# Optimization experiments

Hardware: AMD Instinct MI355X
Metric: run time of the kernel (lower is better)

## Reference

```python
import jax, jax.numpy as jnp
import numpy as np

RADIUS = 2                 # soft detection radius (init kwarg)
NMS_RADIUS = 2             # hardcoded in detect_keypoints: simple_nms(scores, 2)
TOP_K = 4096
TEMPERATURE = 0.1
KSIZE = 2 * RADIUS + 1     # 5
KK = KSIZE * KSIZE         # 25


def _hw_grid(dtype):
    # flatten order j = dy*KSIZE + dx ; entry = (x_off, y_off)  (torch's [:, [1,0]])
    lin = jnp.linspace(-RADIUS, RADIUS, KSIZE, dtype=dtype)
    gx, gy = jnp.meshgrid(lin, lin)  # 'xy': gx[dy,dx]=lin[dx], gy[dy,dx]=lin[dy]
    return jnp.stack([gx, gy], axis=-1).reshape(-1, 2)  # (KK, 2)


def _maxpool(x, r):
    k = 2 * r + 1
    return jax.lax.reduce_window(x, -jnp.inf, jax.lax.max,
                                 (1, 1, k, k), (1, 1, 1, 1),
                                 ((0, 0), (0, 0), (r, r), (r, r)))


def _simple_nms(scores, r):
    zeros = jnp.zeros_like(scores)
    max_mask = scores == _maxpool(scores, r)
    for _ in range(2):
        supp_mask = _maxpool(max_mask.astype(scores.dtype), r) > 0
        supp_scores = jnp.where(supp_mask, zeros, scores)
        new_max_mask = supp_scores == _maxpool(supp_scores, r)
        max_mask = max_mask | (new_max_mask & ~supp_mask)
    return jnp.where(max_mask, scores, zeros)


def _bilinear_zeros(img, xy):
    # img: (h, w); xy: (K, 2) normalized [-1,1]; align_corners=True, zero padding
    h, w = img.shape
    px = (xy[:, 0] + 1.0) * 0.5 * (w - 1)
    py = (xy[:, 1] + 1.0) * 0.5 * (h - 1)
    x0 = jnp.floor(px); y0 = jnp.floor(py)
    wx1 = px - x0; wx0 = 1.0 - wx1
    wy1 = py - y0; wy0 = 1.0 - wy1
    def tap(xi, yi, wgt):
        valid = (xi >= 0) & (xi < w) & (yi >= 0) & (yi < h)
        xc = jnp.clip(xi, 0, w - 1).astype(jnp.int32)
        yc = jnp.clip(yi, 0, h - 1).astype(jnp.int32)
        return jnp.where(valid, img[yc, xc], 0.0) * wgt
    return (tap(x0, y0, wx0 * wy0) + tap(x0 + 1, y0, wx1 * wy0)
            + tap(x0, y0 + 1, wx0 * wy1) + tap(x0 + 1, y0 + 1, wx1 * wy1))


def _dkd_forward(scores_map):
    b, c, h, w = scores_map.shape
    dtype = scores_map.dtype
    scores_nograd = jax.lax.stop_gradient(scores_map)

    nms_scores = _simple_nms(scores_nograd, NMS_RADIUS)
    # zero out border band of width RADIUS
    ybad = (jnp.arange(h) < RADIUS) | (jnp.arange(h) >= h - RADIUS)
    xbad = (jnp.arange(w) < RADIUS) | (jnp.arange(w) >= w - RADIUS)
    border = ybad[:, None] | xbad[None, :]
    nms_scores = jnp.where(border[None, None], 0.0, nms_scores)

    # top-k over flattened score map (per image)
    _, idx = jax.lax.top_k(nms_scores.reshape(b, -1), TOP_K)  # (b, K)
    ix = idx % w
    iy = idx // w

    # patch gather == unfold(scores_map) + gather, done sparsely with zero pad
    padded = jnp.pad(scores_map[:, 0], ((0, 0), (RADIUS, RADIUS), (RADIUS, RADIUS)))
    off = jnp.arange(KSIZE)
    ys = iy[:, :, None] + off[None, None, :]           # (b, K, KSIZE)
    xs = ix[:, :, None] + off[None, None, :]
    bidx = jnp.arange(b)[:, None, None, None]
    patch_scores = padded[bidx, ys[:, :, :, None], xs[:, :, None, :]]  # (b,K,KSIZE,KSIZE)
    patch_scores = patch_scores.reshape(b, TOP_K, KK)

    hw_grid = _hw_grid(dtype)                          # (KK, 2)
    max_v = jax.lax.stop_gradient(patch_scores.max(axis=-1, keepdims=True))
    x_exp = jnp.exp((patch_scores - max_v) / TEMPERATURE)   # (b,K,KK)
    x_exp_sum = x_exp.sum(axis=-1, keepdims=True)            # (b,K,1)
    xy_residual = jnp.einsum('bkp,pd->bkd', x_exp, hw_grid) / x_exp_sum  # (b,K,2)
    hw_dist2 = (((hw_grid[None, None] - xy_residual[:, :, None]) / RADIUS) ** 2).sum(-1)
    scoredispersity = (x_exp * hw_dist2).sum(-1) / x_exp_sum[..., 0]     # (b,K)

    keypoints_xy_nms = jnp.stack([ix, iy], axis=-1).astype(dtype)
    wh = jnp.array([w - 1, h - 1], dtype=dtype)
    keypoints_xy = (keypoints_xy_nms + xy_residual) / wh * 2.0 - 1.0     # (b,K,2)

    kptscore = jax.vmap(_bilinear_zeros)(scores_map[:, 0], keypoints_xy)  # (b,K)
    return keypoints_xy, kptscore, scoredispersity


def setup_inputs() -> dict:
    key = jax.random.key(0)
    scores_map = jax.random.uniform(key, (8, 1, 1024, 1024), dtype=jnp.float32)
    return {"scores_map": scores_map}


def reference(scores_map):
    # matches torch forward: (keypoints, kptscores, scoredispersitys)
    return _dkd_forward(scores_map)
```

## Files before the change

### kernel.cpp

```cpp
#include <hip/hip_runtime.h>
#include <stdint.h>

namespace {

constexpr int B = 8;
constexpr int H = 1024;
constexpr int W = 1024;
constexpr int TOPK = 4096;
constexpr int CAND_CAP = 131072;
constexpr int SEL_CAP = 16384;
constexpr int LIST_CAP = 320;
constexpr int HIST_N = 32768;
constexpr int NCHUNK = 32;
constexpr int NHB = 48;

constexpr int RROWS = 92;
constexpr int NG = 22;
constexpr int STR = 88;
constexpr int MW4 = 4;
constexpr int NSTRIP = 11;
constexpr int NUNIT = NG * NSTRIP;

constexpr int RK_ME = 256;
constexpr int RK_CH = 1024;

constexpr size_t OFF_CNT   = 0;
constexpr size_t OFF_GHIST = 4096;
constexpr size_t OFF_RANK  = OFF_GHIST + (size_t)B * HIST_N * 4;
constexpr size_t OFF_SEL   = OFF_RANK + (size_t)B * SEL_CAP * 4;
constexpr size_t OFF_TOPK  = OFF_SEL + (size_t)B * SEL_CAP * 8;
constexpr size_t OFF_CAND  = OFF_TOPK + (size_t)B * TOPK * 8;
constexpr size_t MEMSET_BYTES = OFF_RANK + (size_t)B * SEL_CAP * 4;

__device__ __forceinline__ float max5(float a, float b, float c, float d, float e) {
  return fmaxf(fmaxf(fmaxf(a, b), fmaxf(c, d)), e);
}
__device__ __forceinline__ float4 ld4(const float* p) {
  return *reinterpret_cast<const float4*>(p);
}

template <int PASS>
__device__ __forceinline__ void score_pass(
    int u, int x0, int y0, const float* __restrict__ S,
    const uint32_t* __restrict__ SUP, uint32_t* __restrict__ MA,
    uint64_t* list, uint32_t* cnt_loc, uint64_t* cand, uint32_t* cand_count, int b) {
  const int G = u % NG, s = u / NG;
  const int r0 = 2 + 8 * s;
  const int gx0 = x0 - 12 + 4 * G;
  uint32_t colm = 0;
#pragma unroll
  for (int j = 0; j < 4; ++j)
    if ((unsigned)(gx0 + j) < (unsigned)W) colm |= 1u << j;
  const int p = 4 * G - 4;
  const int pw = (p < 0) ? 0 : (p >> 5);
  const int psh = (p < 0) ? 0 : (p & 31);
  const int pls = (p < 0) ? -p : 0;

  float4 hw[5], cw[5];
  uint32_t sn[5];
#pragma unroll
  for (int k = 0; k < 12; ++k) {
    const int rr = r0 - 2 + k;
    const float* rowp = S + rr * STR + 4 * G;
    float4 d = ld4(rowp);
    float4 a = (G > 0) ? ld4(rowp - 4) : d;
    float4 e = (G < NG - 1) ? ld4(rowp + 4) : d;
    uint32_t supn = 0;
    if (PASS != 0) {
      const uint32_t* srow = SUP + rr * MW4;
      uint64_t X = (uint64_t)srow[pw] | ((uint64_t)srow[pw + 1] << 32);
      uint64_t win = pls ? (X << pls) : (X >> psh);
      if (win & 0x001u) a.x = 0.f;
      if (win & 0x002u) a.y = 0.f;
      if (win & 0x004u) a.z = 0.f;
      if (win & 0x008u) a.w = 0.f;
      if (win & 0x010u) d.x = 0.f;
      if (win & 0x020u) d.y = 0.f;
      if (win & 0x040u) d.z = 0.f;
      if (win & 0x080u) d.w = 0.f;
      if (win & 0x100u) e.x = 0.f;
      if (win & 0x200u) e.y = 0.f;
      if (win & 0x400u) e.z = 0.f;
      if (win & 0x800u) e.w = 0.f;
      supn = (uint32_t)(win >> 4) & 0xFu;
    }
    float4 hm;
    hm.x = max5(a.z, a.w, d.x, d.y, d.z);
    hm.y = max5(a.w, d.x, d.y, d.z, d.w);
    hm.z = max5(d.x, d.y, d.z, d.w, e.x);
    hm.w = max5(d.y, d.z, d.w, e.x, e.y);
    hw[k % 5] = hm;
    cw[k % 5] = d;
    sn[k % 5] = supn;
    if (k >= 4) {
      const int rq = r0 + k - 4;
      const int gy = y0 - 12 + rq;
      float4 vm;
      vm.x = max5(hw[0].x, hw[1].x, hw[2].x, hw[3].x, hw[4].x);
      vm.y = max5(hw[0].y, hw[1].y, hw[2].y, hw[3].y, hw[4].y);
      vm.z = max5(hw[0].z, hw[1].z, hw[2].z, hw[3].z, hw[4].z);
      vm.w = max5(hw[0].w, hw[1].w, hw[2].w, hw[3].w, hw[4].w);
      float4 c = cw[(k + 3) % 5];
      uint32_t nm = (uint32_t)(c.x == vm.x) | ((uint32_t)(c.y == vm.y) << 1) |
                    ((uint32_t)(c.z == vm.z) << 2) | ((uint32_t)(c.w == vm.w) << 3);
      nm &= ((unsigned)gy < (unsigned)H) ? colm : 0u;
      const int widx = rq * MW4 + (G >> 3);
      const int shift = 4 * (G & 7);
      if (PASS == 0) {
        if (nm) atomicOr(&MA[widx], nm << shift);
      } else if (PASS == 1) {
        uint32_t v = nm & ~sn[(k + 3) % 5];
        if (v) atomicOr(&MA[widx], v << shift);
      } else {
        uint32_t fin = ((MA[widx] >> shift) & 0xFu) | (nm & ~sn[(k + 3) % 5]);
        if (fin && G >= 3 && G < 19 && rq >= 12 && rq < 76 && gy >= 2 && gy < H - 2) {
#pragma unroll
          for (int j = 0; j < 4; ++j) {
            if ((fin >> j) & 1u) {
              int gx = gx0 + j;
              if (gx >= 2 && gx < W - 2) {
                float sval = S[rq * STR + 4 * G + j];
                if (sval > 0.0f) {
                  uint32_t bits = __float_as_uint(sval);
                  uint32_t flat = (uint32_t)(gy * W + gx);
                  uint64_t key = ((uint64_t)bits << 32) | (uint64_t)(0xFFFFFFFFu - flat);
                  uint32_t pos = atomicAdd(cnt_loc, 1u);
                  if (pos < (uint32_t)LIST_CAP) {
                    list[pos] = key;
                  } else {
                    uint32_t pp = atomicAdd(&cand_count[b], 1u);
                    if (pp < (uint32_t)CAND_CAP) cand[(size_t)b * CAND_CAP + pp] = key;
                  }
                }
              }
            }
          }
        }
      }
    }
  }
}

__device__ __forceinline__ void dilate_pass(int u, int x0, int y0,
                                            const uint32_t* __restrict__ MIN_,
                                            uint32_t* __restrict__ SOUT) {
  const int G = u % NG, s = u / NG;
  const int r0 = 2 + 8 * s;
  const int gx0 = x0 - 12 + 4 * G;
  uint32_t colm = 0;
#pragma unroll
  for (int j = 0; j < 4; ++j)
    if ((unsigned)(gx0 + j) < (unsigned)W) colm |= 1u << j;
  const int p = 4 * G - 2;
  const int pw = (p < 0) ? 0 : (p >> 5);
  const int psh = (p < 0) ? 0 : (p & 31);
  const int pls = (p < 0) ? -p : 0;
  uint32_t ring[5];
#pragma unroll
  for (int k = 0; k < 12; ++k) {
    const int rr = r0 - 2 + k;
    const uint32_t* srow = MIN_ + rr * MW4;
    uint64_t X = (uint64_t)srow[pw] | ((uint64_t)srow[pw + 1] << 32);
    uint64_t win = pls ? (X << pls) : (X >> psh);
    uint64_t t = win | (win >> 1) | (win >> 2) | (win >> 3) | (win >> 4);
    ring[k % 5] = (uint32_t)t & 0xFu;
    if (k >= 4) {
      const int rq = r0 + k - 4;
      const int gy = y0 - 12 + rq;
      uint32_t nib = ring[0] | ring[1] | ring[2] | ring[3] | ring[4];
      nib &= ((unsigned)gy < (unsigned)H) ? colm : 0u;
      if (nib) atomicOr(&SOUT[rq * MW4 + (G >> 3)], nib << (4 * (G & 7)));
    }
  }
}

__global__ void __launch_bounds__(256, 4) k_nms(const float* __restrict__ scores,
                                                uint64_t* __restrict__ cand,
                                                uint32_t* __restrict__ cand_count) {
  __shared__ float S[RROWS * STR];
  __shared__ uint32_t MAs[RROWS * MW4];
  __shared__ uint32_t SP1[RROWS * MW4];
  __shared__ uint32_t SP2[RROWS * MW4];
  __shared__ uint64_t list[LIST_CAP];
  __shared__ uint32_t cnt_loc, base_g;
  const int b = blockIdx.z;
  const int x0 = blockIdx.x * 64, y0 = blockIdx.y * 64;
  const int tid = threadIdx.x;
  const float* img = scores + (size_t)b * H * W;
  if (tid == 0) cnt_loc = 0;

  for (int u = tid; u < RROWS * NG; u += 256) {
    int r = u / NG, G = u % NG;
    int gy = y0 - 12 + r, gx = x0 - 12 + 4 * G;
    float4 v;
    if ((unsigned)gy < (unsigned)H && (unsigned)gx < (unsigned)W)
      v = ld4(img + (size_t)gy * W + gx);
    else
      v = make_float4(-INFINITY, -INFINITY, -INFINITY, -INFINITY);
    *reinterpret_cast<float4*>(&S[r * STR + 4 * G]) = v;
  }
  for (int i = tid; i < RROWS * MW4; i += 256) {
    MAs[i] = 0;
    SP1[i] = 0;
    SP2[i] = 0;
  }
  __syncthreads();
  if (tid < NUNIT)
    score_pass<0>(tid, x0, y0, S, nullptr, MAs, nullptr, nullptr, nullptr, nullptr, b);
  __syncthreads();
  if (tid < NUNIT) dilate_pass(tid, x0, y0, MAs, SP1);
  __syncthreads();
  if (tid < NUNIT)
    score_pass<1>(tid, x0, y0, S, SP1, MAs, nullptr, nullptr, nullptr, nullptr, b);
  __syncthreads();
  if (tid < NUNIT) dilate_pass(tid, x0, y0, MAs, SP2);
  __syncthreads();
  if (tid < NUNIT)
    score_pass<2>(tid, x0, y0, S, SP2, MAs, list, &cnt_loc, cand, cand_count, b);
  __syncthreads();
  uint32_t nblk = cnt_loc;
  uint32_t nmain = nblk < (uint32_t)LIST_CAP ? nblk : (uint32_t)LIST_CAP;
  if (tid == 0) base_g = atomicAdd(&cand_count[b], nmain);
  __syncthreads();
  uint32_t bg = base_g;
  for (uint32_t i = tid; i < nmain; i += 256) {
    uint32_t pp = bg + i;
    if (pp < (uint32_t)CAND_CAP) cand[(size_t)b * CAND_CAP + pp] = list[i];
  }
}

__global__ void __launch_bounds__(256) k_hist(const uint64_t* __restrict__ cand,
                                              const uint32_t* __restrict__ cand_count,
                                              uint32_t* __restrict__ ghist) {
  const int b = blockIdx.y;
  uint32_t n = cand_count[b];
  if (n > (uint32_t)CAND_CAP) n = CAND_CAP;
  uint32_t* gh = ghist + (size_t)b * HIST_N;
  const uint64_t* cb = cand + (size_t)b * CAND_CAP;
  const int lane = threadIdx.x & 63;
  for (uint32_t i = blockIdx.x * 256 + threadIdx.x;; i += NHB * 256) {
    bool valid = i < n;
    uint64_t act = __ballot(valid);
    if (!act) break;
    uint32_t bkt = 0;
    if (valid) bkt = (uint32_t)(cb[i] >> 47);
    uint64_t peers = act;
#pragma unroll
    for (int bit = 0; bit < 15; ++bit) {
      uint64_t bb = __ballot((bkt >> bit) & 1u);
      peers &= ((bkt >> bit) & 1u) ? bb : ~bb;
    }
    if (valid && (__ffsll((unsigned long long)peers) - 1) == lane)
      atomicAdd(&gh[bkt], (uint32_t)__popcll((unsigned long long)peers));
  }
}

__global__ void __launch_bounds__(256) k_chunksum(const uint32_t* __restrict__ ghist,
                                                  uint32_t* __restrict__ gchunk) {
  const int b = blockIdx.y, c = blockIdx.x;
  const uint32_t* gh = ghist + (size_t)b * HIST_N + c * 1024;
  uint32_t s = 0;
#pragma unroll
  for (int j = 0; j < 4; ++j) s += gh[threadIdx.x + 256 * j];
#pragma unroll
  for (int m = 1; m < 64; m <<= 1) s += __shfl_xor(s, m);
  __shared__ uint32_t red[4];
  if ((threadIdx.x & 63) == 0) red[threadIdx.x >> 6] = s;
  __syncthreads();
  if (threadIdx.x == 0) gchunk[b * NCHUNK + c] = red[0] + red[1] + red[2] + red[3];
}

__global__ void __launch_bounds__(1024) k_findthr(const uint32_t* __restrict__ ghist,
                                                  const uint32_t* __restrict__ gchunk,
                                                  uint64_t* __restrict__ thr_key) {
  __shared__ uint32_t ch[NCHUNK];
  __shared__ uint32_t h[1024];
  __shared__ int shCC;
  __shared__ uint32_t sh_above;
  const int b = blockIdx.x, t = threadIdx.x;
  if (t < NCHUNK) ch[t] = gchunk[b * NCHUNK + t];
  __syncthreads();
  if (t == 0) {
    uint32_t run = 0;
    int CC = -1;
    uint32_t above = 0;
    for (int c = NCHUNK - 1; c >= 0; --c) {
      uint32_t nrun = run + ch[c];
      if (run < (uint32_t)TOPK && nrun >= (uint32_t)TOPK) { CC = c; above = run; }
      run = nrun;
    }
    if (run < (uint32_t)TOPK) CC = -1;
    shCC = CC;
    sh_above = above;
  }
  __syncthreads();
  const int CC = shCC;
  if (CC < 0) {
    if (t == 0) thr_key[b] = 0ull;
    return;
  }
  const uint32_t above = sh_above;
  h[t] = ghist[(size_t)b * HIST_N + CC * 1024 + t];
  __syncthreads();
  for (int d = 1; d < 1024; d <<= 1) {
    uint32_t v = (t + d < 1024) ? h[t + d] : 0u;
    __syncthreads();
    h[t] += v;
    __syncthreads();
  }
  uint32_t cum = above + h[t];
  uint32_t cumn = (t + 1 < 1024) ? above + h[t + 1] : above;
  if (cum >= (uint32_t)TOPK && cumn < (uint32_t)TOPK)
    thr_key[b] = (uint64_t)(CC * 1024 + t) << 47;
}

__global__ void __launch_bounds__(1024) k_compact(const uint64_t* __restrict__ cand,
                                                  const uint32_t* __restrict__ cand_count,
                                                  const uint64_t* __restrict__ thr_key,
                                                  uint64_t* __restrict__ sel,
                                                  uint32_t* __restrict__ sel_count) {
  __shared__ uint64_t list[1024];
  __shared__ uint32_t cnt_loc;
  __shared__ uint32_t base_g;
  const int b = blockIdx.y;
  uint32_t n = cand_count[b];
  if (n > (uint32_t)CAND_CAP) n = CAND_CAP;
  const int tid = threadIdx.x;
  if (tid == 0) cnt_loc = 0;
  __syncthreads();
  uint32_t i = blockIdx.x * 1024 + tid;
  if (i < n) {
    uint64_t key = cand[(size_t)b * CAND_CAP + i];
    if (key >= thr_key[b]) {
      uint32_t pos = atomicAdd(&cnt_loc, 1u);
      list[pos] = key;
    }
  }
  __syncthreads();
  uint32_t nblk = cnt_loc;
  if (tid == 0 && nblk > 0) base_g = atomicAdd(&sel_count[b], nblk);
  __syncthreads();
  if (nblk > 0 && (uint32_t)tid < nblk) {
    uint32_t pp = base_g + tid;
    if (pp < (uint32_t)SEL_CAP) sel[(size_t)b * SEL_CAP + pp] = list[tid];
  }
}

__global__ void __launch_bounds__(RK_ME) k_rank_part(const uint64_t* __restrict__ sel,
                                                     const uint32_t* __restrict__ sel_count,
                                                     uint32_t* __restrict__ rankg) {
  __shared__ uint64_t keys[RK_CH];
  const int b = blockIdx.z;
  uint32_t n = sel_count[b];
  if (n > (uint32_t)SEL_CAP) n = SEL_CAP;
  const uint32_t me0 = blockIdx.x * RK_ME;
  const uint32_t c0 = blockIdx.y * RK_CH;
  if (me0 >= n || c0 >= n) return;
  const uint64_t* sb = sel + (size_t)b * SEL_CAP;
  uint32_t clen = n - c0;
  if (clen > (uint32_t)RK_CH) clen = RK_CH;
  for (uint32_t i = threadIdx.x; i < clen; i += RK_ME) keys[i] = sb[c0 + i];
  __syncthreads();
  const uint32_t me = me0 + threadIdx.x;
  if (me >= n) return;
  const uint64_t kme = sb[me];
  uint32_t rank = 0;
  uint32_t i = 0;
  for (; i + 8 <= clen; i += 8) {
    rank += (keys[i] > kme);
    rank += (keys[i + 1] > kme);
    rank += (keys[i + 2] > kme);
    rank += (keys[i + 3] > kme);
    rank += (keys[i + 4] > kme);
    rank += (keys[i + 5] > kme);
    rank += (keys[i + 6] > kme);
    rank += (keys[i + 7] > kme);
  }
  for (; i < clen; ++i) rank += (keys[i] > kme);
  if (rank) atomicAdd(&rankg[(size_t)b * SEL_CAP + me], rank);
}

__global__ void __launch_bounds__(256) k_scatter(const uint64_t* __restrict__ sel,
                                                 const uint32_t* __restrict__ sel_count,
                                                 const uint32_t* __restrict__ rankg,
                                                 uint64_t* __restrict__ topk) {
  const int b = blockIdx.y;
  uint32_t n = sel_count[b];
  if (n > (uint32_t)SEL_CAP) n = SEL_CAP;
  uint32_t i = blockIdx.x * 256 + threadIdx.x;
  if (i >= n) return;
  uint32_t r = rankg[(size_t)b * SEL_CAP + i];
  if (r < (uint32_t)TOPK) topk[(size_t)b * TOPK + r] = sel[(size_t)b * SEL_CAP + i];
}

__global__ void __launch_bounds__(256) k_refine(const float* __restrict__ scores,
                                                const uint64_t* __restrict__ topk,
                                                float* __restrict__ out) {
  int gid = blockIdx.x * 256 + threadIdx.x;
  int kp = gid >> 3, ln = gid & 7;
  const int b = kp / TOPK;
  const int k = kp % TOPK;
  uint64_t key = topk[(size_t)b * TOPK + k];
  uint32_t flat = 0xFFFFFFFFu - (uint32_t)(key & 0xFFFFFFFFull);
  if (flat >= (uint32_t)(H * W)) flat = 0;
  const int ix = (int)(flat % W);
  const int iy = (int)(flat / W);
  const float* img = scores + (size_t)b * H * W;

  const int nt = (ln == 0) ? 4 : 3;
  float v[4];
  float mymax = -INFINITY;
#pragma unroll
  for (int i = 0; i < 4; ++i) {
    if (i < nt) {
      int t = ln + 8 * i;
      int y = iy + t / 5 - 2, x = ix + t % 5 - 2;
      float val = ((unsigned)x < (unsigned)W && (unsigned)y < (unsigned)H)
                      ? img[(size_t)y * W + x] : 0.0f;
      v[i] = val;
      mymax = fmaxf(mymax, val);
    }
  }
#pragma unroll
  for (int m = 1; m < 8; m <<= 1) mymax = fmaxf(mymax, __shfl_xor(mymax, m));
  float e[4];
  float sum = 0.f, sx = 0.f, sy = 0.f;
#pragma unroll
  for (int i = 0; i < 4; ++i) {
    if (i < nt) {
      int t = ln + 8 * i;
      float ev = expf((v[i] - mymax) / 0.1f);
      e[i] = ev;
      sum += ev;
      sx += ev * (float)(t % 5 - 2);
      sy += ev * (float)(t / 5 - 2);
    }
  }
#pragma unroll
  for (int m = 1; m < 8; m <<= 1) {
    sum += __shfl_xor(sum, m);
    sx += __shfl_xor(sx, m);
    sy += __shfl_xor(sy, m);
  }
  float rx = sx / sum, ry = sy / sum;
  float dsp = 0.f;
#pragma unroll
  for (int i = 0; i < 4; ++i) {
    if (i < nt) {
      int t = ln + 8 * i;
      float dx = ((float)(t % 5 - 2) - rx) * 0.5f;
      float dy = ((float)(t / 5 - 2) - ry) * 0.5f;
      dsp += e[i] * (dx * dx + dy * dy);
    }
  }
#pragma unroll
  for (int m = 1; m < 8; m <<= 1) dsp += __shfl_xor(dsp, m);
  if (ln != 0) return;
  dsp /= sum;
  float kx = ((float)ix + rx) / 1023.0f * 2.0f - 1.0f;
  float ky = ((float)iy + ry) / 1023.0f * 2.0f - 1.0f;
  float px = (kx + 1.0f) * 0.5f * 1023.0f;
  float py = (ky + 1.0f) * 0.5f * 1023.0f;
  float x0f = floorf(px), y0f = floorf(py);
  float wx1 = px - x0f, wx0 = 1.0f - wx1;
  float wy1 = py - y0f, wy0 = 1.0f - wy1;
  int x0 = (int)x0f, y0 = (int)y0f;
  float sc = 0.0f;
  {
    int xs[2] = {x0, x0 + 1};
    int ys[2] = {y0, y0 + 1};
    float wxs[2] = {wx0, wx1};
    float wys[2] = {wy0, wy1};
#pragma unroll
    for (int yy = 0; yy < 2; ++yy)
#pragma unroll
      for (int xx = 0; xx < 2; ++xx) {
        int xi = xs[xx], yi = ys[yy];
        bool valid = (xi >= 0 && xi < W && yi >= 0 && yi < H);
        int xc = min(max(xi, 0), W - 1);
        int yc = min(max(yi, 0), H - 1);
        float vv = valid ? img[(size_t)yc * W + xc] : 0.0f;
        sc += vv * (wxs[xx] * wys[yy]);
      }
  }
  out[((size_t)b * TOPK + k) * 2 + 0] = kx;
  out[((size_t)b * TOPK + k) * 2 + 1] = ky;
  out[(size_t)B * TOPK * 2 + (size_t)b * TOPK + k] = sc;
  out[(size_t)B * TOPK * 3 + (size_t)b * TOPK + k] = dsp;
}

}

extern "C" void kernel_launch(void* const* d_in, const int* in_sizes, int n_in,
                              void* d_out, int out_size, void* d_ws, size_t ws_size,
                              hipStream_t stream) {
  const float* scores = (const float*)d_in[0];
  float* out = (float*)d_out;
  char* ws = (char*)d_ws;

  uint32_t* cnt = (uint32_t*)(ws + OFF_CNT);
  uint32_t* cand_count = cnt;
  uint32_t* sel_count  = cnt + 8;
  uint64_t* thr_key    = (uint64_t*)(cnt + 16);
  uint32_t* gchunk     = cnt + 256;
  uint32_t* ghist = (uint32_t*)(ws + OFF_GHIST);
  uint32_t* rankg = (uint32_t*)(ws + OFF_RANK);
  uint64_t* sel  = (uint64_t*)(ws + OFF_SEL);
  uint64_t* topk = (uint64_t*)(ws + OFF_TOPK);
  uint64_t* cand = (uint64_t*)(ws + OFF_CAND);

  hipMemsetAsync(ws + OFF_CNT, 0, MEMSET_BYTES, stream);

  k_nms<<<dim3(W / 64, H / 64, B), 256, 0, stream>>>(scores, cand, cand_count);
  k_hist<<<dim3(NHB, B), 256, 0, stream>>>(cand, cand_count, ghist);
  k_chunksum<<<dim3(NCHUNK, B), 256, 0, stream>>>(ghist, gchunk);
  k_findthr<<<B, 1024, 0, stream>>>(ghist, gchunk, thr_key);
  k_compact<<<dim3(CAND_CAP / 1024, B), 1024, 0, stream>>>(cand, cand_count, thr_key, sel, sel_count);
  k_rank_part<<<dim3(SEL_CAP / RK_ME, SEL_CAP / RK_CH, B), RK_ME, 0, stream>>>(sel, sel_count, rankg);
  k_scatter<<<dim3(SEL_CAP / 256, B), 256, 0, stream>>>(sel, sel_count, rankg, topk);
  k_refine<<<(B * TOPK * 8) / 256, 256, 0, stream>>>(scores, topk, out);
}
```

Measured before the change: 225.7 us.

## Fuse NMS dilation into score passes, histogram in NMS, merge rank and scatter

Folds the separate mask-dilation passes into the score passes, so the NMS kernel runs three passes with fewer barriers and one fewer shared mask buffer. It also builds the score histogram inside the NMS kernel with global atomics, which removes the separate histogram and chunk-sum kernels. The threshold search now does a two-level scan inside a single kernel. The partial-rank and scatter kernels become one rank kernel that loops over all chunks, so the rank buffer and its memset are no longer needed. The cost is per-candidate global atomics on the histogram from the NMS kernel and fewer parallel blocks in the rank step.

```diff
diff --git a/kernel.cpp b/kernel.cpp
--- a/kernel.cpp
+++ b/kernel.cpp
@@ -11,8 +11,6 @@
 constexpr int SEL_CAP = 16384;
 constexpr int LIST_CAP = 320;
 constexpr int HIST_N = 32768;
-constexpr int NCHUNK = 32;
-constexpr int NHB = 48;
 
 constexpr int RROWS = 92;
 constexpr int NG = 22;
@@ -21,7 +19,6 @@
 constexpr int NSTRIP = 11;
 constexpr int NUNIT = NG * NSTRIP;
 
-constexpr int RK_ME = 256;
 constexpr int RK_CH = 1024;
 
 constexpr size_t OFF_CNT   = 0;
@@ -30,7 +27,7 @@
 constexpr size_t OFF_SEL   = OFF_RANK + (size_t)B * SEL_CAP * 4;
 constexpr size_t OFF_TOPK  = OFF_SEL + (size_t)B * SEL_CAP * 8;
 constexpr size_t OFF_CAND  = OFF_TOPK + (size_t)B * TOPK * 8;
-constexpr size_t MEMSET_BYTES = OFF_RANK + (size_t)B * SEL_CAP * 4;
+constexpr size_t MEMSET_BYTES = OFF_RANK;
 
 __device__ __forceinline__ float max5(float a, float b, float c, float d, float e) {
   return fmaxf(fmaxf(fmaxf(a, b), fmaxf(c, d)), e);
@@ -42,8 +39,9 @@
 template <int PASS>
 __device__ __forceinline__ void score_pass(
     int u, int x0, int y0, const float* __restrict__ S,
-    const uint32_t* __restrict__ SUP, uint32_t* __restrict__ MA,
-    uint64_t* list, uint32_t* cnt_loc, uint64_t* cand, uint32_t* cand_count, int b) {
+    const uint32_t* __restrict__ MIN_, uint32_t* __restrict__ MOUT,
+    uint64_t* list, uint32_t* cnt_loc, uint64_t* cand, uint32_t* cand_count,
+    uint32_t* __restrict__ ghist, int b) {
   const int G = u % NG, s = u / NG;
   const int r0 = 2 + 8 * s;
   const int gx0 = x0 - 12 + 4 * G;
@@ -51,85 +49,102 @@
 #pragma unroll
   for (int j = 0; j < 4; ++j)
     if ((unsigned)(gx0 + j) < (unsigned)W) colm |= 1u << j;
-  const int p = 4 * G - 4;
-  const int pw = (p < 0) ? 0 : (p >> 5);
-  const int psh = (p < 0) ? 0 : (p & 31);
-  const int pls = (p < 0) ? -p : 0;
+
+  const int p2 = 4 * G - 6;
+  const int pw2 = (p2 < 0) ? 0 : (p2 >> 5);
+  const int psh2 = (p2 < 0) ? 0 : (p2 & 31);
+  const int pls2 = (p2 < 0) ? -p2 : 0;
 
   float4 hw[5], cw[5];
-  uint32_t sn[5];
-#pragma unroll
-  for (int k = 0; k < 12; ++k) {
-    const int rr = r0 - 2 + k;
-    const float* rowp = S + rr * STR + 4 * G;
-    float4 d = ld4(rowp);
-    float4 a = (G > 0) ? ld4(rowp - 4) : d;
-    float4 e = (G < NG - 1) ? ld4(rowp + 4) : d;
-    uint32_t supn = 0;
+  uint32_t snr[5], mor[5], cnb[5];
+  constexpr int NK = (PASS == 0) ? 12 : 16;
+#pragma unroll
+  for (int k = 0; k < NK; ++k) {
     if (PASS != 0) {
-      const uint32_t* srow = SUP + rr * MW4;
-      uint64_t X = (uint64_t)srow[pw] | ((uint64_t)srow[pw + 1] << 32);
-      uint64_t win = pls ? (X << pls) : (X >> psh);
-      if (win & 0x001u) a.x = 0.f;
-      if (win & 0x002u) a.y = 0.f;
-      if (win & 0x004u) a.z = 0.f;
-      if (win & 0x008u) a.w = 0.f;
-      if (win & 0x010u) d.x = 0.f;
-      if (win & 0x020u) d.y = 0.f;
-      if (win & 0x040u) d.z = 0.f;
-      if (win & 0x080u) d.w = 0.f;
-      if (win & 0x100u) e.x = 0.f;
-      if (win & 0x200u) e.y = 0.f;
-      if (win & 0x400u) e.z = 0.f;
-      if (win & 0x800u) e.w = 0.f;
-      supn = (uint32_t)(win >> 4) & 0xFu;
-    }
-    float4 hm;
-    hm.x = max5(a.z, a.w, d.x, d.y, d.z);
-    hm.y = max5(a.w, d.x, d.y, d.z, d.w);
-    hm.z = max5(d.x, d.y, d.z, d.w, e.x);
-    hm.w = max5(d.y, d.z, d.w, e.x, e.y);
-    hw[k % 5] = hm;
-    cw[k % 5] = d;
-    sn[k % 5] = supn;
-    if (k >= 4) {
-      const int rq = r0 + k - 4;
-      const int gy = y0 - 12 + rq;
-      float4 vm;
-      vm.x = max5(hw[0].x, hw[1].x, hw[2].x, hw[3].x, hw[4].x);
-      vm.y = max5(hw[0].y, hw[1].y, hw[2].y, hw[3].y, hw[4].y);
-      vm.z = max5(hw[0].z, hw[1].z, hw[2].z, hw[3].z, hw[4].z);
-      vm.w = max5(hw[0].w, hw[1].w, hw[2].w, hw[3].w, hw[4].w);
-      float4 c = cw[(k + 3) % 5];
-      uint32_t nm = (uint32_t)(c.x == vm.x) | ((uint32_t)(c.y == vm.y) << 1) |
-                    ((uint32_t)(c.z == vm.z) << 2) | ((uint32_t)(c.w == vm.w) << 3);
-      nm &= ((unsigned)gy < (unsigned)H) ? colm : 0u;
-      const int widx = rq * MW4 + (G >> 3);
-      const int shift = 4 * (G & 7);
-      if (PASS == 0) {
-        if (nm) atomicOr(&MA[widx], nm << shift);
-      } else if (PASS == 1) {
-        uint32_t v = nm & ~sn[(k + 3) % 5];
-        if (v) atomicOr(&MA[widx], v << shift);
-      } else {
-        uint32_t fin = ((MA[widx] >> shift) & 0xFu) | (nm & ~sn[(k + 3) % 5]);
-        if (fin && G >= 3 && G < 19 && rq >= 12 && rq < 76 && gy >= 2 && gy < H - 2) {
-#pragma unroll
-          for (int j = 0; j < 4; ++j) {
-            if ((fin >> j) & 1u) {
-              int gx = gx0 + j;
-              if (gx >= 2 && gx < W - 2) {
-                float sval = S[rq * STR + 4 * G + j];
-                if (sval > 0.0f) {
-                  uint32_t bits = __float_as_uint(sval);
-                  uint32_t flat = (uint32_t)(gy * W + gx);
-                  uint64_t key = ((uint64_t)bits << 32) | (uint64_t)(0xFFFFFFFFu - flat);
-                  uint32_t pos = atomicAdd(cnt_loc, 1u);
-                  if (pos < (uint32_t)LIST_CAP) {
-                    list[pos] = key;
-                  } else {
-                    uint32_t pp = atomicAdd(&cand_count[b], 1u);
-                    if (pp < (uint32_t)CAND_CAP) cand[(size_t)b * CAND_CAP + pp] = key;
+      const int mr = r0 - 4 + k;
+      uint32_t morrow = 0, cnib = 0;
+      if ((unsigned)mr < (unsigned)RROWS) {
+        const uint32_t* srow = MIN_ + mr * MW4;
+        uint64_t X = (uint64_t)srow[pw2] | ((uint64_t)srow[pw2 + 1] << 32);
+        uint64_t win = pls2 ? (X << pls2) : (X >> psh2);
+        uint64_t t5 = win | (win >> 1) | (win >> 2) | (win >> 3) | (win >> 4);
+        morrow = (uint32_t)t5 & 0xFFFu;
+        cnib = (uint32_t)(win >> 6) & 0xFu;
+      }
+      mor[k % 5] = morrow;
+      cnb[k % 5] = cnib;
+    }
+    const int ks = (PASS == 0) ? k : k - 4;
+    if (ks >= 0) {
+      const int sr = r0 - 2 + ks;
+      uint32_t supp = 0;
+      if (PASS != 0) supp = mor[0] | mor[1] | mor[2] | mor[3] | mor[4];
+      const float* rowp = S + sr * STR + 4 * G;
+      float4 d = ld4(rowp);
+      float4 a = (G > 0) ? ld4(rowp - 4) : d;
+      float4 e = (G < NG - 1) ? ld4(rowp + 4) : d;
+      if (PASS != 0) {
+        if (supp & 0x001u) a.x = 0.f;
+        if (supp & 0x002u) a.y = 0.f;
+        if (supp & 0x004u) a.z = 0.f;
+        if (supp & 0x008u) a.w = 0.f;
+        if (supp & 0x010u) d.x = 0.f;
+        if (supp & 0x020u) d.y = 0.f;
+        if (supp & 0x040u) d.z = 0.f;
+        if (supp & 0x080u) d.w = 0.f;
+        if (supp & 0x100u) e.x = 0.f;
+        if (supp & 0x200u) e.y = 0.f;
+        if (supp & 0x400u) e.z = 0.f;
+        if (supp & 0x800u) e.w = 0.f;
+      }
+      float4 hm;
+      hm.x = max5(a.z, a.w, d.x, d.y, d.z);
+      hm.y = max5(a.w, d.x, d.y, d.z, d.w);
+      hm.z = max5(d.x, d.y, d.z, d.w, e.x);
+      hm.w = max5(d.y, d.z, d.w, e.x, e.y);
+      hw[ks % 5] = hm;
+      cw[ks % 5] = d;
+      snr[ks % 5] = (supp >> 4) & 0xFu;
+      if (ks >= 4) {
+        const int rq = r0 - 4 + ks;
+        const int gy = y0 - 12 + rq;
+        float4 vm;
+        vm.x = max5(hw[0].x, hw[1].x, hw[2].x, hw[3].x, hw[4].x);
+        vm.y = max5(hw[0].y, hw[1].y, hw[2].y, hw[3].y, hw[4].y);
+        vm.z = max5(hw[0].z, hw[1].z, hw[2].z, hw[3].z, hw[4].z);
+        vm.w = max5(hw[0].w, hw[1].w, hw[2].w, hw[3].w, hw[4].w);
+        float4 c = cw[(ks + 3) % 5];
+        uint32_t nm = (uint32_t)(c.x == vm.x) | ((uint32_t)(c.y == vm.y) << 1) |
+                      ((uint32_t)(c.z == vm.z) << 2) | ((uint32_t)(c.w == vm.w) << 3);
+        nm &= ((unsigned)gy < (unsigned)H) ? colm : 0u;
+        const int widx = rq * MW4 + (G >> 3);
+        const int shift = 4 * (G & 7);
+        if (PASS == 0) {
+          if (nm) atomicOr(&MOUT[widx], nm << shift);
+        } else if (PASS == 1) {
+          uint32_t fin = cnb[ks % 5] | (nm & ~snr[(ks + 3) % 5]);
+          if (fin) atomicOr(&MOUT[widx], fin << shift);
+        } else {
+          uint32_t fin = cnb[ks % 5] | (nm & ~snr[(ks + 3) % 5]);
+          if (fin && G >= 3 && G < 19 && rq >= 12 && rq < 76 && gy >= 2 && gy < H - 2) {
+#pragma unroll
+            for (int j = 0; j < 4; ++j) {
+              if ((fin >> j) & 1u) {
+                int gx = gx0 + j;
+                if (gx >= 2 && gx < W - 2) {
+                  float sval = S[rq * STR + 4 * G + j];
+                  if (sval > 0.0f) {
+                    uint32_t bits = __float_as_uint(sval);
+                    atomicAdd(&ghist[(size_t)b * HIST_N + (bits >> 15)], 1u);
+                    uint32_t flat = (uint32_t)(gy * W + gx);
+                    uint64_t key = ((uint64_t)bits << 32) | (uint64_t)(0xFFFFFFFFu - flat);
+                    uint32_t pos = atomicAdd(cnt_loc, 1u);
+                    if (pos < (uint32_t)LIST_CAP) {
+                      list[pos] = key;
+                    } else {
+                      uint32_t pp = atomicAdd(&cand_count[b], 1u);
+                      if (pp < (uint32_t)CAND_CAP) cand[(size_t)b * CAND_CAP + pp] = key;
+                    }
                   }
                 }
               }
@@ -141,46 +156,13 @@
   }
 }
 
-__device__ __forceinline__ void dilate_pass(int u, int x0, int y0,
-                                            const uint32_t* __restrict__ MIN_,
-                                            uint32_t* __restrict__ SOUT) {
-  const int G = u % NG, s = u / NG;
-  const int r0 = 2 + 8 * s;
-  const int gx0 = x0 - 12 + 4 * G;
-  uint32_t colm = 0;
-#pragma unroll
-  for (int j = 0; j < 4; ++j)
-    if ((unsigned)(gx0 + j) < (unsigned)W) colm |= 1u << j;
-  const int p = 4 * G - 2;
-  const int pw = (p < 0) ? 0 : (p >> 5);
-  const int psh = (p < 0) ? 0 : (p & 31);
-  const int pls = (p < 0) ? -p : 0;
-  uint32_t ring[5];
-#pragma unroll
-  for (int k = 0; k < 12; ++k) {
-    const int rr = r0 - 2 + k;
-    const uint32_t* srow = MIN_ + rr * MW4;
-    uint64_t X = (uint64_t)srow[pw] | ((uint64_t)srow[pw + 1] << 32);
-    uint64_t win = pls ? (X << pls) : (X >> psh);
-    uint64_t t = win | (win >> 1) | (win >> 2) | (win >> 3) | (win >> 4);
-    ring[k % 5] = (uint32_t)t & 0xFu;
-    if (k >= 4) {
-      const int rq = r0 + k - 4;
-      const int gy = y0 - 12 + rq;
-      uint32_t nib = ring[0] | ring[1] | ring[2] | ring[3] | ring[4];
-      nib &= ((unsigned)gy < (unsigned)H) ? colm : 0u;
-      if (nib) atomicOr(&SOUT[rq * MW4 + (G >> 3)], nib << (4 * (G & 7)));
-    }
-  }
-}
-
 __global__ void __launch_bounds__(256, 4) k_nms(const float* __restrict__ scores,
                                                 uint64_t* __restrict__ cand,
-                                                uint32_t* __restrict__ cand_count) {
+                                                uint32_t* __restrict__ cand_count,
+                                                uint32_t* __restrict__ ghist) {
   __shared__ float S[RROWS * STR];
-  __shared__ uint32_t MAs[RROWS * MW4];
-  __shared__ uint32_t SP1[RROWS * MW4];
-  __shared__ uint32_t SP2[RROWS * MW4];
+  __shared__ uint32_t M0s[RROWS * MW4];
+  __shared__ uint32_t M1s[RROWS * MW4];
   __shared__ uint64_t list[LIST_CAP];
   __shared__ uint32_t cnt_loc, base_g;
   const int b = blockIdx.z;
@@ -200,23 +182,21 @@
     *reinterpret_cast<float4*>(&S[r * STR + 4 * G]) = v;
   }
   for (int i = tid; i < RROWS * MW4; i += 256) {
-    MAs[i] = 0;
-    SP1[i] = 0;
-    SP2[i] = 0;
+    M0s[i] = 0;
+    M1s[i] = 0;
   }
   __syncthreads();
   if (tid < NUNIT)
-    score_pass<0>(tid, x0, y0, S, nullptr, MAs, nullptr, nullptr, nullptr, nullptr, b);
-  __syncthreads();
-  if (tid < NUNIT) dilate_pass(tid, x0, y0, MAs, SP1);
+    score_pass<0>(tid, x0, y0, S, nullptr, M0s, nullptr, nullptr, nullptr, nullptr,
+                  nullptr, b);
   __syncthreads();
   if (tid < NUNIT)
-    score_pass<1>(tid, x0, y0, S, SP1, MAs, nullptr, nullptr, nullptr, nullptr, b);
-  __syncthreads();
-  if (tid < NUNIT) dilate_pass(tid, x0, y0, MAs, SP2);
+    score_pass<1>(tid, x0, y0, S, M0s, M1s, nullptr, nullptr, nullptr, nullptr,
+                  nullptr, b);
   __syncthreads();
   if (tid < NUNIT)
-    score_pass<2>(tid, x0, y0, S, SP2, MAs, list, &cnt_loc, cand, cand_count, b);
+    score_pass<2>(tid, x0, y0, S, M1s, nullptr, list, &cnt_loc, cand, cand_count,
+                  ghist, b);
   __syncthreads();
   uint32_t nblk = cnt_loc;
   uint32_t nmain = nblk < (uint32_t)LIST_CAP ? nblk : (uint32_t)LIST_CAP;
@@ -229,78 +209,18 @@
   }
 }
 
-__global__ void __launch_bounds__(256) k_hist(const uint64_t* __restrict__ cand,
-                                              const uint32_t* __restrict__ cand_count,
-                                              uint32_t* __restrict__ ghist) {
-  const int b = blockIdx.y;
-  uint32_t n = cand_count[b];
-  if (n > (uint32_t)CAND_CAP) n = CAND_CAP;
-  uint32_t* gh = ghist + (size_t)b * HIST_N;
-  const uint64_t* cb = cand + (size_t)b * CAND_CAP;
-  const int lane = threadIdx.x & 63;
-  for (uint32_t i = blockIdx.x * 256 + threadIdx.x;; i += NHB * 256) {
-    bool valid = i < n;
-    uint64_t act = __ballot(valid);
-    if (!act) break;
-    uint32_t bkt = 0;
-    if (valid) bkt = (uint32_t)(cb[i] >> 47);
-    uint64_t peers = act;
-#pragma unroll
-    for (int bit = 0; bit < 15; ++bit) {
-      uint64_t bb = __ballot((bkt >> bit) & 1u);
-      peers &= ((bkt >> bit) & 1u) ? bb : ~bb;
-    }
-    if (valid && (__ffsll((unsigned long long)peers) - 1) == lane)
-      atomicAdd(&gh[bkt], (uint32_t)__popcll((unsigned long long)peers));
-  }
-}
-
-__global__ void __launch_bounds__(256) k_chunksum(const uint32_t* __restrict__ ghist,
-                                                  uint32_t* __restrict__ gchunk) {
-  const int b = blockIdx.y, c = blockIdx.x;
-  const uint32_t* gh = ghist + (size_t)b * HIST_N + c * 1024;
+__global__ void __launch_bounds__(1024) k_findthr(const uint32_t* __restrict__ ghist,
+                                                  uint64_t* __restrict__ thr_key) {
+  __shared__ uint32_t h[1024];
+  const int b = blockIdx.x, t = threadIdx.x;
+  const uint32_t* gh = ghist + (size_t)b * HIST_N + t * 32;
   uint32_t s = 0;
 #pragma unroll
-  for (int j = 0; j < 4; ++j) s += gh[threadIdx.x + 256 * j];
-#pragma unroll
-  for (int m = 1; m < 64; m <<= 1) s += __shfl_xor(s, m);
-  __shared__ uint32_t red[4];
-  if ((threadIdx.x & 63) == 0) red[threadIdx.x >> 6] = s;
-  __syncthreads();
-  if (threadIdx.x == 0) gchunk[b * NCHUNK + c] = red[0] + red[1] + red[2] + red[3];
-}
-
-__global__ void __launch_bounds__(1024) k_findthr(const uint32_t* __restrict__ ghist,
-                                                  const uint32_t* __restrict__ gchunk,
-                                                  uint64_t* __restrict__ thr_key) {
-  __shared__ uint32_t ch[NCHUNK];
-  __shared__ uint32_t h[1024];
-  __shared__ int shCC;
-  __shared__ uint32_t sh_above;
-  const int b = blockIdx.x, t = threadIdx.x;
-  if (t < NCHUNK) ch[t] = gchunk[b * NCHUNK + t];
-  __syncthreads();
-  if (t == 0) {
-    uint32_t run = 0;
-    int CC = -1;
-    uint32_t above = 0;
-    for (int c = NCHUNK - 1; c >= 0; --c) {
-      uint32_t nrun = run + ch[c];
-      if (run < (uint32_t)TOPK && nrun >= (uint32_t)TOPK) { CC = c; above = run; }
-      run = nrun;
-    }
-    if (run < (uint32_t)TOPK) CC = -1;
-    shCC = CC;
-    sh_above = above;
-  }
-  __syncthreads();
-  const int CC = shCC;
-  if (CC < 0) {
-    if (t == 0) thr_key[b] = 0ull;
-    return;
-  }
-  const uint32_t above = sh_above;
-  h[t] = ghist[(size_t)b * HIST_N + CC * 1024 + t];
+  for (int j = 0; j < 8; ++j) {
+    uint4 v = *reinterpret_cast<const uint4*>(gh + 4 * j);
+    s += v.x + v.y + v.z + v.w;
+  }
+  h[t] = s;
   __syncthreads();
   for (int d = 1; d < 1024; d <<= 1) {
     uint32_t v = (t + d < 1024) ? h[t + d] : 0u;
@@ -308,10 +228,21 @@
     h[t] += v;
     __syncthreads();
   }
-  uint32_t cum = above + h[t];
-  uint32_t cumn = (t + 1 < 1024) ? above + h[t + 1] : above;
-  if (cum >= (uint32_t)TOPK && cumn < (uint32_t)TOPK)
-    thr_key[b] = (uint64_t)(CC * 1024 + t) << 47;
+  uint32_t cum = h[t];
+  uint32_t nxt = (t < 1023) ? h[t + 1] : 0u;
+  if (t == 0 && cum < (uint32_t)TOPK) thr_key[b] = 0ull;
+  if (cum >= (uint32_t)TOPK && nxt < (uint32_t)TOPK) {
+    uint32_t run = nxt;
+    int thrb = t * 32;
+    for (int j = 31; j >= 0; --j) {
+      run += gh[j];
+      if (run >= (uint32_t)TOPK) {
+        thrb = t * 32 + j;
+        break;
+      }
+    }
+    thr_key[b] = (uint64_t)thrb << 47;
+  }
 }
 
 __global__ void __launch_bounds__(1024) k_compact(const uint64_t* __restrict__ cand,
@@ -346,51 +277,38 @@
   }
 }
 
-__global__ void __launch_bounds__(RK_ME) k_rank_part(const uint64_t* __restrict__ sel,
-                                                     const uint32_t* __restrict__ sel_count,
-                                                     uint32_t* __restrict__ rankg) {
+__global__ void __launch_bounds__(256) k_rank(const uint64_t* __restrict__ sel,
+                                              const uint32_t* __restrict__ sel_count,
+                                              uint64_t* __restrict__ topk) {
   __shared__ uint64_t keys[RK_CH];
-  const int b = blockIdx.z;
-  uint32_t n = sel_count[b];
-  if (n > (uint32_t)SEL_CAP) n = SEL_CAP;
-  const uint32_t me0 = blockIdx.x * RK_ME;
-  const uint32_t c0 = blockIdx.y * RK_CH;
-  if (me0 >= n || c0 >= n) return;
-  const uint64_t* sb = sel + (size_t)b * SEL_CAP;
-  uint32_t clen = n - c0;
-  if (clen > (uint32_t)RK_CH) clen = RK_CH;
-  for (uint32_t i = threadIdx.x; i < clen; i += RK_ME) keys[i] = sb[c0 + i];
-  __syncthreads();
-  const uint32_t me = me0 + threadIdx.x;
-  if (me >= n) return;
-  const uint64_t kme = sb[me];
-  uint32_t rank = 0;
-  uint32_t i = 0;
-  for (; i + 8 <= clen; i += 8) {
-    rank += (keys[i] > kme);
-    rank += (keys[i + 1] > kme);
-    rank += (keys[i + 2] > kme);
-    rank += (keys[i + 3] > kme);
-    rank += (keys[i + 4] > kme);
-    rank += (keys[i + 5] > kme);
-    rank += (keys[i + 6] > kme);
-    rank += (keys[i + 7] > kme);
-  }
-  for (; i < clen; ++i) rank += (keys[i] > kme);
-  if (rank) atomicAdd(&rankg[(size_t)b * SEL_CAP + me], rank);
-}
-
-__global__ void __launch_bounds__(256) k_scatter(const uint64_t* __restrict__ sel,
-                                                 const uint32_t* __restrict__ sel_count,
-                                                 const uint32_t* __restrict__ rankg,
-                                                 uint64_t* __restrict__ topk) {
   const int b = blockIdx.y;
   uint32_t n = sel_count[b];
   if (n > (uint32_t)SEL_CAP) n = SEL_CAP;
-  uint32_t i = blockIdx.x * 256 + threadIdx.x;
-  if (i >= n) return;
-  uint32_t r = rankg[(size_t)b * SEL_CAP + i];
-  if (r < (uint32_t)TOPK) topk[(size_t)b * TOPK + r] = sel[(size_t)b * SEL_CAP + i];
+  if (blockIdx.x * 256u >= n) return;
+  const uint64_t* sb = sel + (size_t)b * SEL_CAP;
+  const uint32_t me = blockIdx.x * 256u + threadIdx.x;
+  const uint64_t kme = (me < n) ? sb[me] : 0ull;
+  uint32_t rank = 0;
+  for (uint32_t c0 = 0; c0 < n; c0 += RK_CH) {
+    uint32_t clen = n - c0;
+    if (clen > (uint32_t)RK_CH) clen = RK_CH;
+    __syncthreads();
+    for (uint32_t i = threadIdx.x; i < clen; i += 256) keys[i] = sb[c0 + i];
+    __syncthreads();
+    uint32_t i = 0;
+    for (; i + 8 <= clen; i += 8) {
+      rank += (keys[i] > kme);
+      rank += (keys[i + 1] > kme);
+      rank += (keys[i + 2] > kme);
+      rank += (keys[i + 3] > kme);
+      rank += (keys[i + 4] > kme);
+      rank += (keys[i + 5] > kme);
+      rank += (keys[i + 6] > kme);
+      rank += (keys[i + 7] > kme);
+    }
+    for (; i < clen; ++i) rank += (keys[i] > kme);
+  }
+  if (me < n && rank < (uint32_t)TOPK) topk[(size_t)b * TOPK + rank] = kme;
 }
 
 __global__ void __launch_bounds__(256) k_refine(const float* __restrict__ scores,
@@ -502,21 +420,17 @@
   uint32_t* cand_count = cnt;
   uint32_t* sel_count  = cnt + 8;
   uint64_t* thr_key    = (uint64_t*)(cnt + 16);
-  uint32_t* gchunk     = cnt + 256;
   uint32_t* ghist = (uint32_t*)(ws + OFF_GHIST);
-  uint32_t* rankg = (uint32_t*)(ws + OFF_RANK);
   uint64_t* sel  = (uint64_t*)(ws + OFF_SEL);
   uint64_t* topk = (uint64_t*)(ws + OFF_TOPK);
   uint64_t* cand = (uint64_t*)(ws + OFF_CAND);
 
   hipMemsetAsync(ws + OFF_CNT, 0, MEMSET_BYTES, stream);
 
-  k_nms<<<dim3(W / 64, H / 64, B), 256, 0, stream>>>(scores, cand, cand_count);
-  k_hist<<<dim3(NHB, B), 256, 0, stream>>>(cand, cand_count, ghist);
-  k_chunksum<<<dim3(NCHUNK, B), 256, 0, stream>>>(ghist, gchunk);
-  k_findthr<<<B, 1024, 0, stream>>>(ghist, gchunk, thr_key);
-  k_compact<<<dim3(CAND_CAP / 1024, B), 1024, 0, stream>>>(cand, cand_count, thr_key, sel, sel_count);
-  k_rank_part<<<dim3(SEL_CAP / RK_ME, SEL_CAP / RK_CH, B), RK_ME, 0, stream>>>(sel, sel_count, rankg);
-  k_scatter<<<dim3(SEL_CAP / 256, B), 256, 0, stream>>>(sel, sel_count, rankg, topk);
+  k_nms<<<dim3(W / 64, H / 64, B), 256, 0, stream>>>(scores, cand, cand_count, ghist);
+  k_findthr<<<B, 1024, 0, stream>>>(ghist, thr_key);
+  k_compact<<<dim3(CAND_CAP / 1024, B), 1024, 0, stream>>>(cand, cand_count, thr_key,
+                                                           sel, sel_count);
+  k_rank<<<dim3(SEL_CAP / 256, B), 256, 0, stream>>>(sel, sel_count, topk);
   k_refine<<<(B * TOPK * 8) / 256, 256, 0, stream>>>(scores, topk, out);
 }
```

After: 630.2 us. 2.79x slower.
